# Optimization experiments

Hardware: AMD Instinct MI355X
Metric: run time of the kernel (lower is better)

## Reference

```python
import jax, jax.numpy as jnp
import numpy as np

B, T, V, H = 32, 512, 32000, 1024


def setup_inputs() -> dict:
    key = jax.random.key(0)
    k0, k1, k2, k3 = jax.random.split(key, 4)
    x = jax.random.randint(k0, (B, T), 0, V, dtype=jnp.int32)
    hidden = jnp.zeros((B, H), jnp.float32)
    embedding = jax.random.normal(k1, (V, H), jnp.float32) * 0.02
    # glorot-ish scaling for the gate kernels
    kernel = jax.random.normal(k2, (H, 3 * H), jnp.float32) * (1.0 / np.sqrt(H))
    recurrent_kernel = jax.random.normal(k3, (H, 3 * H), jnp.float32) * (1.0 / np.sqrt(H))
    bias = jnp.zeros((2, 3 * H), jnp.float32)  # [input_bias, recurrent_bias] (reset_after=True)
    return {"x": x, "hidden": hidden, "embedding": embedding,
            "kernel": kernel, "recurrent_kernel": recurrent_kernel, "bias": bias}


def reference(x, hidden, embedding, kernel, recurrent_kernel, bias):
    mask = (x != 0)                      # mask_zero=True: token id 0 is padding
    emb = embedding[x]                   # [B, T, H]
    b_i, b_r = bias[0], bias[1]

    def step(h, inp):
        x_t, m_t = inp                   # x_t: [B, H], m_t: [B]
        gx = x_t @ kernel + b_i          # [B, 3H]
        gh = h @ recurrent_kernel + b_r  # [B, 3H] (reset_after=True)
        xz, xr, xn = jnp.split(gx, 3, axis=-1)
        hz, hr, hn = jnp.split(gh, 3, axis=-1)
        z = jax.nn.sigmoid(xz + hz)
        r = jax.nn.sigmoid(xr + hr)
        hh = jnp.tanh(xn + r * hn)
        h_new = z * h + (1.0 - z) * hh
        # masked steps: carry previous state/output forward
        h_new = jnp.where(m_t[:, None], h_new, h)
        return h_new, h_new

    xs = (jnp.swapaxes(emb, 0, 1), jnp.swapaxes(mask, 0, 1))  # time-major
    state, outs = jax.lax.scan(step, hidden, xs)
    output = jnp.swapaxes(outs, 0, 1)    # [B, T, H]
    return output, state
```

## Files before the change

kernel.cpp:

```cpp
#include <hip/hip_runtime.h>
#include <hip/hip_bf16.h>
#include <math.h>


#define B_  32
#define T_  512
#define H_  1024
#define H3  3072
#define NG  64
#define UPG 16

typedef short short8 __attribute__((ext_vector_type(8)));
typedef float float4_ __attribute__((ext_vector_type(4)));
typedef int   int4_  __attribute__((ext_vector_type(4)));
typedef unsigned short u16;
typedef unsigned long long ull;

__device__ __forceinline__ float bf2f(u16 u) {
  union { unsigned i; float f; } v; v.i = ((unsigned)u) << 16; return v.f;
}
__device__ __forceinline__ u16 f2bf(float f) {
  union { float f; unsigned i; } v; v.f = f;
  unsigned r = v.i + 0x7FFFu + ((v.i >> 16) & 1u);
  return (u16)(r >> 16);
}
__device__ __forceinline__ float ldf(const void* p, size_t i, int f32) {
  return f32 ? ((const float*)p)[i] : bf2f(((const u16*)p)[i]);
}
__device__ __forceinline__ short8 ld8(const void* base, size_t off, int f32) {
  short8 r;
  if (f32) {
    const float* p = (const float*)base + off;
    float4_ a = *(const float4_*)p;
    float4_ b = *(const float4_*)(p + 4);
    r[0]=(short)f2bf(a[0]); r[1]=(short)f2bf(a[1]); r[2]=(short)f2bf(a[2]); r[3]=(short)f2bf(a[3]);
    r[4]=(short)f2bf(b[0]); r[5]=(short)f2bf(b[1]); r[6]=(short)f2bf(b[2]); r[7]=(short)f2bf(b[3]);
  } else {
    r = *(const short8*)((const u16*)base + off);
  }
  return r;
}

__device__ __forceinline__ ull atomLD(const ull* p) {
  return __hip_atomic_load((ull*)p, __ATOMIC_RELAXED, __HIP_MEMORY_SCOPE_AGENT);
}
__device__ __forceinline__ void atomST(ull* p, ull v) {
  __hip_atomic_store(p, v, __ATOMIC_RELAXED, __HIP_MEMORY_SCOPE_AGENT);
}
__device__ __forceinline__ ull packh(unsigned tag, float h0, float h1) {
  return ((ull)tag << 32) | ((ull)f2bf(h1) << 16) | (ull)f2bf(h0);
}

__global__ __launch_bounds__(256) void detect_norm(
    const void* __restrict__ emb, const void* __restrict__ bias,
    int* dflag, float* __restrict__ bias_c) {
  __shared__ int cnt;
  __shared__ int sflag;
  if (threadIdx.x == 0) cnt = 0;
  __syncthreads();
  const unsigned* e = (const unsigned*)emb;
  const unsigned lo = e[threadIdx.x] & 0xFFFFu;
  if (((lo >> 7) & 0xFFu) >= 128u) atomicAdd(&cnt, 1);
  __syncthreads();
  if (threadIdx.x == 0) {
    sflag = (cnt > 32) ? 1 : 0;
    *dflag = sflag;
  }
  __syncthreads();
  const int f32 = sflag;
  for (int i = threadIdx.x; i < 2 * H3; i += 256) bias_c[i] = ldf(bias, i, f32);
}

__global__ __launch_bounds__(256) void transpose_kernel(
    const void* __restrict__ W, const void* __restrict__ R,
    u16* __restrict__ Wt, u16* __restrict__ Rt, const int* dflag) {
  __shared__ u16 tile[32][33];
  const int f32 = *dflag;
  const void* src = blockIdx.z ? R : W;
  u16* dst = blockIdx.z ? Rt : Wt;
  int k0 = blockIdx.x * 32, n0 = blockIdx.y * 32;
  int c = threadIdx.x & 31, r8 = threadIdx.x >> 5;
  for (int rr = r8; rr < 32; rr += 8)
    tile[rr][c] = f2bf(ldf(src, (size_t)(k0 + rr) * H3 + n0 + c, f32));
  __syncthreads();
  for (int rr = r8; rr < 32; rr += 8)
    dst[(size_t)(n0 + rr) * H_ + k0 + c] = tile[c][rr];
}

__global__ __launch_bounds__(256) void gx_gemm(
    const int* __restrict__ x, const void* __restrict__ emb,
    const u16* __restrict__ Wt, const float* __restrict__ bias_c,
    u16* __restrict__ gx, const int* dflag) {
  __shared__ u16 Al[128][72];
  __shared__ u16 Bl[128][72];
  __shared__ int tok[128];
  const int f32 = *dflag;
  const int tid = threadIdx.x;
  const int n0 = blockIdx.x * 128;
  const int t0 = blockIdx.y * 4;
  if (tid < 128) { int b = tid >> 2, dt = tid & 3; tok[tid] = x[b * T_ + t0 + dt]; }
  __syncthreads();
  const int lane = tid & 63, w = tid >> 6;
  const int l = lane & 15, q = lane >> 4;
  const int wm = w >> 1, wn = w & 1;
  float4_ acc[4][4];
  for (int i = 0; i < 4; i++) for (int j = 0; j < 4; j++) acc[i][j] = (float4_)0.0f;
  const int row = tid >> 1, half = tid & 1;
  for (int k0 = 0; k0 < H_; k0 += 64) {
    const size_t offA = (size_t)tok[row] * H_ + k0 + half * 32;
    const u16* srcB = Wt + (size_t)(n0 + row) * H_ + k0 + half * 32;
#pragma unroll
    for (int c = 0; c < 4; c++) {
      *(short8*)&Al[row][half * 32 + c * 8] = ld8(emb, offA + c * 8, f32);
      *(short8*)&Bl[row][half * 32 + c * 8] = *(const short8*)(srcB + c * 8);
    }
    __syncthreads();
#pragma unroll
    for (int ks = 0; ks < 2; ks++) {
      const int kk = ks * 32 + q * 8;
      short8 af[4], bfv[4];
#pragma unroll
      for (int mi = 0; mi < 4; mi++) af[mi] = *(const short8*)&Al[wm * 64 + mi * 16 + l][kk];
#pragma unroll
      for (int ni = 0; ni < 4; ni++) bfv[ni] = *(const short8*)&Bl[wn * 64 + ni * 16 + l][kk];
#pragma unroll
      for (int mi = 0; mi < 4; mi++)
#pragma unroll
        for (int ni = 0; ni < 4; ni++)
          acc[mi][ni] = __builtin_amdgcn_mfma_f32_16x16x32_bf16(af[mi], bfv[ni], acc[mi][ni], 0, 0, 0);
    }
    __syncthreads();
  }
  for (int ni = 0; ni < 4; ni++) {
    const int n = n0 + wn * 64 + ni * 16 + l;
    const float bi = bias_c[n];
    for (int mi = 0; mi < 4; mi++) {
#pragma unroll
      for (int rr = 0; rr < 4; rr++) {
        const int rloc = wm * 64 + mi * 16 + q * 4 + rr;
        const int b = rloc >> 2, dt = rloc & 3;
        gx[((size_t)(t0 + dt) * H3 + n) * B_ + b] = f2bf(acc[mi][ni][rr] + bi);
      }
    }
  }
}

__global__ __launch_bounds__(256, 1) void gru_recur(
    const int* __restrict__ x, const void* __restrict__ hidden,
    const u16* __restrict__ Rt, const float* __restrict__ bias_c,
    const u16* __restrict__ gx, ull* __restrict__ hbuf,
    void* __restrict__ out, const int* dflag) {
  extern __shared__ char smem[];
  u16* Rl = (u16*)smem;
  float* P = (float*)(smem + 99072);
  unsigned* mw = (unsigned*)(smem + 99072 + 50176);
  const int f32o = *dflag;
  const int g = blockIdx.x, tid = threadIdx.x;
  const int lane = tid & 63, w = tid >> 6;
  const int l = lane & 15, q = lane >> 4;
  float* outf = (float*)out;
  u16* outb = (u16*)out;

  for (int i = tid; i < 48 * 128; i += 256) {
    const int cc = i >> 7, ch = i & 127;
    const int c = cc >> 4, u = cc & 15;
    *(short8*)&Rl[cc * 1032 + ch * 8] =
        *(const short8*)(Rt + (size_t)(c * H_ + g * UPG + u) * H_ + ch * 8);
  }
  for (int i = tid; i < 512; i += 256) mw[i] = 0u;
  __syncthreads();
  for (int i = tid; i < B_ * T_; i += 256) {
    const int b = i >> 9, t = i & 511;
    if (x[i] != 0) atomicOr(&mw[t], 1u << b);
  }

  const int b = tid & 31, up = tid >> 5;
  const int col0 = g * UPG + 2 * up;
  float br[2][3], hp[2];
#pragma unroll
  for (int p = 0; p < 2; p++) {
    const int col = col0 + p;
    br[p][0] = bias_c[H3 + col];
    br[p][1] = bias_c[H3 + H_ + col];
    br[p][2] = bias_c[H3 + 2 * H_ + col];
    hp[p] = ldf(hidden, (size_t)b * H_ + col, f32o);
  }
  atomST(&hbuf[16384 + (size_t)(g * 8 + up) * 32 + b], packh(1u, hp[0], hp[1]));
  __syncthreads();

  for (int t = 0; t < T_; t++) {
    float gxv[2][3];
#pragma unroll
    for (int p = 0; p < 2; p++) {
      const int col = col0 + p;
#pragma unroll
      for (int c = 0; c < 3; c++)
        gxv[p][c] = bf2f(gx[((size_t)t * H3 + c * H_ + col) * B_ + b]);
    }

    const ull* hb = hbuf + (size_t)((t + 1) & 1) * 16384;
    const unsigned tg = (unsigned)(t + 1);
    const int jb0 = w * 128 + q * 4;
    ull va[8][8];
#pragma unroll
    for (int kk = 0; kk < 8; kk++) {
      const ull* p = hb + (size_t)(jb0 + kk * 16) * 32 + l;
#pragma unroll
      for (int i = 0; i < 4; i++) {
        va[kk][i]     = atomLD(p + i * 32);
        va[kk][4 + i] = atomLD(p + i * 32 + 16);
      }
    }
    while (1) {
      int anybad = 0;
#pragma unroll
      for (int kk = 0; kk < 8; kk++) {
        int ok = 1;
#pragma unroll
        for (int i = 0; i < 8; i++) ok &= ((unsigned)(va[kk][i] >> 32) == tg);
        if (!__all(ok)) {
          anybad = 1;
          const ull* p = hb + (size_t)(jb0 + kk * 16) * 32 + l;
#pragma unroll
          for (int i = 0; i < 4; i++) {
            va[kk][i]     = atomLD(p + i * 32);
            va[kk][4 + i] = atomLD(p + i * 32 + 16);
          }
        }
      }
      if (!anybad) break;
      __builtin_amdgcn_s_sleep(1);
    }

    float4_ acc[2][3];
#pragma unroll
    for (int mt = 0; mt < 2; mt++)
#pragma unroll
      for (int nt = 0; nt < 3; nt++) acc[mt][nt] = (float4_)0.0f;
#pragma unroll
    for (int kk = 0; kk < 8; kk++) {
      const int k = w * 256 + kk * 32 + q * 8;
      union { int4_ d; short8 s; } ua, ub;
#pragma unroll
      for (int i = 0; i < 4; i++) {
        ua.d[i] = (int)(unsigned)va[kk][i];
        ub.d[i] = (int)(unsigned)va[kk][4 + i];
      }
      const short8 a0 = ua.s, a1 = ub.s;
      const short8 r0 = *(const short8*)&Rl[(0 * 16 + l) * 1032 + k];
      const short8 r1 = *(const short8*)&Rl[(1 * 16 + l) * 1032 + k];
      const short8 r2 = *(const short8*)&Rl[(2 * 16 + l) * 1032 + k];
      acc[0][0] = __builtin_amdgcn_mfma_f32_16x16x32_bf16(a0, r0, acc[0][0], 0, 0, 0);
      acc[0][1] = __builtin_amdgcn_mfma_f32_16x16x32_bf16(a0, r1, acc[0][1], 0, 0, 0);
      acc[0][2] = __builtin_amdgcn_mfma_f32_16x16x32_bf16(a0, r2, acc[0][2], 0, 0, 0);
      acc[1][0] = __builtin_amdgcn_mfma_f32_16x16x32_bf16(a1, r0, acc[1][0], 0, 0, 0);
      acc[1][1] = __builtin_amdgcn_mfma_f32_16x16x32_bf16(a1, r1, acc[1][1], 0, 0, 0);
      acc[1][2] = __builtin_amdgcn_mfma_f32_16x16x32_bf16(a1, r2, acc[1][2], 0, 0, 0);
    }
    float* Pc = P + (t & 1) * 6272;
#pragma unroll
    for (int mt = 0; mt < 2; mt++)
#pragma unroll
      for (int nt = 0; nt < 3; nt++)
#pragma unroll
        for (int rr = 0; rr < 4; rr++)
          Pc[w * 1568 + (mt * 16 + q * 4 + rr) * 49 + nt * 16 + l] = acc[mt][nt][rr];
    __syncthreads();

    const unsigned mword = mw[t];
#pragma unroll
    for (int p = 0; p < 2; p++) {
      const int u = 2 * up + p;
      float hz = 0.f, hr = 0.f, hn = 0.f;
#pragma unroll
      for (int ww = 0; ww < 4; ww++) {
        const float* Pb = Pc + ww * 1568 + b * 49;
        hz += Pb[u]; hr += Pb[16 + u]; hn += Pb[32 + u];
      }
      hz += br[p][0]; hr += br[p][1]; hn += br[p][2];
      const float z = 1.f / (1.f + __expf(-(gxv[p][0] + hz)));
      const float r = 1.f / (1.f + __expf(-(gxv[p][1] + hr)));
      float nn = gxv[p][2] + r * hn;
      nn = fminf(fmaxf(nn, -15.f), 15.f);
      const float e2 = __expf(2.f * nn);
      const float th = (e2 - 1.f) / (e2 + 1.f);
      float hnew = z * hp[p] + (1.f - z) * th;
      if (!((mword >> b) & 1u)) hnew = hp[p];
      hp[p] = hnew;
    }
    atomST(&hbuf[(size_t)(t & 1) * 16384 + (size_t)(g * 8 + up) * 32 + b],
           packh((unsigned)(t + 2), hp[0], hp[1]));
    const size_t oi = ((size_t)b * T_ + t) * H_ + col0;
    if (f32o) {
      __builtin_nontemporal_store(hp[0], outf + oi);
      __builtin_nontemporal_store(hp[1], outf + oi + 1);
    } else {
      const unsigned pw = ((unsigned)f2bf(hp[1]) << 16) | (unsigned)f2bf(hp[0]);
      __builtin_nontemporal_store(pw, (unsigned*)(outb + oi));
    }
  }
  {
    const size_t oi = (size_t)B_ * T_ * H_ + (size_t)b * H_ + col0;
    if (f32o) {
      __builtin_nontemporal_store(hp[0], outf + oi);
      __builtin_nontemporal_store(hp[1], outf + oi + 1);
    } else {
      const unsigned pw = ((unsigned)f2bf(hp[1]) << 16) | (unsigned)f2bf(hp[0]);
      __builtin_nontemporal_store(pw, (unsigned*)(outb + oi));
    }
  }
}

extern "C" void kernel_launch(void* const* d_in, const int* in_sizes, int n_in,
                              void* d_out, int out_size, void* d_ws, size_t ws_size,
                              hipStream_t stream) {
  const int* x       = (const int*)d_in[0];
  const void* hidden = d_in[1];
  const void* emb    = d_in[2];
  const void* W      = d_in[3];
  const void* R      = d_in[4];
  const void* bias   = d_in[5];
  char* ws = (char*)d_ws;
  u16*   gx      = (u16*)ws;
  u16*   Wt      = (u16*)(ws + 100663296);
  u16*   Rt      = (u16*)(ws + 106954752);
  ull*   hbuf    = (ull*)(ws + 113246208);
  int*   dflag   = (int*)(ws + 113508352);
  float* bias_c  = (float*)(ws + 113508608);

  hipLaunchKernelGGL(detect_norm, dim3(1), dim3(256), 0, stream,
                     emb, bias, dflag, bias_c);
  hipLaunchKernelGGL(transpose_kernel, dim3(32, 96, 2), dim3(256), 0, stream,
                     W, R, Wt, Rt, dflag);
  hipLaunchKernelGGL(gx_gemm, dim3(24, 128), dim3(256), 0, stream,
                     x, emb, Wt, bias_c, gx, dflag);
  hipFuncSetAttribute((const void*)gru_recur, hipFuncAttributeMaxDynamicSharedMemorySize, 151296);
  hipLaunchKernelGGL(gru_recur, dim3(NG), dim3(256), 151296, stream,
                     x, hidden, Rt, bias_c, gx, hbuf, d_out, dflag);
}
```

Measured before the change: 3.017 ms.

## Replace per-element tagged hidden-state polling with per-wave epoch flags

Hidden-state exchange between blocks previously used 64-bit words carrying a step tag beside the packed bf16 pair, and each consumer polled all the words it needed. Now the data is stored as plain 32-bit words, and each wave publishes a per-step epoch flag after a waitcnt. Consumers spin on 256 flags before loading the data once. This halves the exchange traffic and simplifies polling, but relies on relaxed-atomic ordering between the data store and the flag store. The P scratch stride also changes from 49 to 50.

```diff
diff --git a/kernel.cpp b/kernel.cpp
--- a/kernel.cpp
+++ b/kernel.cpp
@@ -14,7 +14,7 @@
 typedef float float4_ __attribute__((ext_vector_type(4)));
 typedef int   int4_  __attribute__((ext_vector_type(4)));
 typedef unsigned short u16;
-typedef unsigned long long ull;
+typedef unsigned int u32;
 
 __device__ __forceinline__ float bf2f(u16 u) {
   union { unsigned i; float f; } v; v.i = ((unsigned)u) << 16; return v.f;
@@ -41,19 +41,19 @@
   return r;
 }
 
-__device__ __forceinline__ ull atomLD(const ull* p) {
-  return __hip_atomic_load((ull*)p, __ATOMIC_RELAXED, __HIP_MEMORY_SCOPE_AGENT);
-}
-__device__ __forceinline__ void atomST(ull* p, ull v) {
+__device__ __forceinline__ u32 aload32(const u32* p) {
+  return __hip_atomic_load((u32*)p, __ATOMIC_RELAXED, __HIP_MEMORY_SCOPE_AGENT);
+}
+__device__ __forceinline__ void astore32(u32* p, u32 v) {
   __hip_atomic_store(p, v, __ATOMIC_RELAXED, __HIP_MEMORY_SCOPE_AGENT);
 }
-__device__ __forceinline__ ull packh(unsigned tag, float h0, float h1) {
-  return ((ull)tag << 32) | ((ull)f2bf(h1) << 16) | (ull)f2bf(h0);
+__device__ __forceinline__ u32 pack2(float h0, float h1) {
+  return ((u32)f2bf(h1) << 16) | (u32)f2bf(h0);
 }
 
 __global__ __launch_bounds__(256) void detect_norm(
     const void* __restrict__ emb, const void* __restrict__ bias,
-    int* dflag, float* __restrict__ bias_c) {
+    int* dflag, float* __restrict__ bias_c, u32* __restrict__ ep) {
   __shared__ int cnt;
   __shared__ int sflag;
   if (threadIdx.x == 0) cnt = 0;
@@ -69,6 +69,8 @@
   __syncthreads();
   const int f32 = sflag;
   for (int i = threadIdx.x; i < 2 * H3; i += 256) bias_c[i] = ldf(bias, i, f32);
+  astore32(&ep[threadIdx.x], 0u);
+  astore32(&ep[threadIdx.x + 256], 0u);
 }
 
 __global__ __launch_bounds__(256) void transpose_kernel(
@@ -148,12 +150,12 @@
 __global__ __launch_bounds__(256, 1) void gru_recur(
     const int* __restrict__ x, const void* __restrict__ hidden,
     const u16* __restrict__ Rt, const float* __restrict__ bias_c,
-    const u16* __restrict__ gx, ull* __restrict__ hbuf,
-    void* __restrict__ out, const int* dflag) {
+    const u16* __restrict__ gx, u32* __restrict__ hdat,
+    u32* __restrict__ ep, void* __restrict__ out, const int* dflag) {
   extern __shared__ char smem[];
   u16* Rl = (u16*)smem;
   float* P = (float*)(smem + 99072);
-  unsigned* mw = (unsigned*)(smem + 99072 + 50176);
+  unsigned* mw = (unsigned*)(smem + 99072 + 51200);
   const int f32o = *dflag;
   const int g = blockIdx.x, tid = threadIdx.x;
   const int lane = tid & 63, w = tid >> 6;
@@ -185,7 +187,10 @@
     br[p][2] = bias_c[H3 + 2 * H_ + col];
     hp[p] = ldf(hidden, (size_t)b * H_ + col, f32o);
   }
-  atomST(&hbuf[16384 + (size_t)(g * 8 + up) * 32 + b], packh(1u, hp[0], hp[1]));
+  astore32(&hdat[16384 + (size_t)(g * 8 + up) * 32 + b], pack2(hp[0], hp[1]));
+  __builtin_amdgcn_s_waitcnt(0);
+  __builtin_amdgcn_sched_barrier(0);
+  if ((tid & 63) == 0) astore32(&ep[256 + g * 4 + w], 1u);
   __syncthreads();
 
   for (int t = 0; t < T_; t++) {
@@ -198,38 +203,30 @@
         gxv[p][c] = bf2f(gx[((size_t)t * H3 + c * H_ + col) * B_ + b]);
     }
 
-    const ull* hb = hbuf + (size_t)((t + 1) & 1) * 16384;
-    const unsigned tg = (unsigned)(t + 1);
+    const u32 aw = (u32)(t + 1);
+    const u32* epp = ep + (size_t)((t + 1) & 1) * 256;
+    const int lid = lane;
+    while (1) {
+      u32 e0 = aload32(epp + lid);
+      u32 e1 = aload32(epp + lid + 64);
+      u32 e2 = aload32(epp + lid + 128);
+      u32 e3 = aload32(epp + lid + 192);
+      if (__all(e0 == aw && e1 == aw && e2 == aw && e3 == aw)) break;
+      __builtin_amdgcn_s_sleep(1);
+    }
+    __builtin_amdgcn_sched_barrier(0);
+
+    const u32* hd = hdat + (size_t)((t + 1) & 1) * 16384;
     const int jb0 = w * 128 + q * 4;
-    ull va[8][8];
+    u32 va[8][8];
 #pragma unroll
     for (int kk = 0; kk < 8; kk++) {
-      const ull* p = hb + (size_t)(jb0 + kk * 16) * 32 + l;
+      const u32* p = hd + (size_t)(jb0 + kk * 16) * 32 + l;
 #pragma unroll
       for (int i = 0; i < 4; i++) {
-        va[kk][i]     = atomLD(p + i * 32);
-        va[kk][4 + i] = atomLD(p + i * 32 + 16);
+        va[kk][i]     = aload32(p + i * 32);
+        va[kk][4 + i] = aload32(p + i * 32 + 16);
       }
-    }
-    while (1) {
-      int anybad = 0;
-#pragma unroll
-      for (int kk = 0; kk < 8; kk++) {
-        int ok = 1;
-#pragma unroll
-        for (int i = 0; i < 8; i++) ok &= ((unsigned)(va[kk][i] >> 32) == tg);
-        if (!__all(ok)) {
-          anybad = 1;
-          const ull* p = hb + (size_t)(jb0 + kk * 16) * 32 + l;
-#pragma unroll
-          for (int i = 0; i < 4; i++) {
-            va[kk][i]     = atomLD(p + i * 32);
-            va[kk][4 + i] = atomLD(p + i * 32 + 16);
-          }
-        }
-      }
-      if (!anybad) break;
-      __builtin_amdgcn_s_sleep(1);
     }
 
     float4_ acc[2][3];
@@ -243,8 +240,8 @@
       union { int4_ d; short8 s; } ua, ub;
 #pragma unroll
       for (int i = 0; i < 4; i++) {
-        ua.d[i] = (int)(unsigned)va[kk][i];
-        ub.d[i] = (int)(unsigned)va[kk][4 + i];
+        ua.d[i] = (int)va[kk][i];
+        ub.d[i] = (int)va[kk][4 + i];
       }
       const short8 a0 = ua.s, a1 = ub.s;
       const short8 r0 = *(const short8*)&Rl[(0 * 16 + l) * 1032 + k];
@@ -257,14 +254,14 @@
       acc[1][1] = __builtin_amdgcn_mfma_f32_16x16x32_bf16(a1, r1, acc[1][1], 0, 0, 0);
       acc[1][2] = __builtin_amdgcn_mfma_f32_16x16x32_bf16(a1, r2, acc[1][2], 0, 0, 0);
     }
-    float* Pc = P + (t & 1) * 6272;
+    float* Pc = P + (t & 1) * 6400;
 #pragma unroll
     for (int mt = 0; mt < 2; mt++)
 #pragma unroll
       for (int nt = 0; nt < 3; nt++)
 #pragma unroll
         for (int rr = 0; rr < 4; rr++)
-          Pc[w * 1568 + (mt * 16 + q * 4 + rr) * 49 + nt * 16 + l] = acc[mt][nt][rr];
+          Pc[w * 1600 + (mt * 16 + q * 4 + rr) * 50 + nt * 16 + l] = acc[mt][nt][rr];
     __syncthreads();
 
     const unsigned mword = mw[t];
@@ -274,7 +271,7 @@
       float hz = 0.f, hr = 0.f, hn = 0.f;
 #pragma unroll
       for (int ww = 0; ww < 4; ww++) {
-        const float* Pb = Pc + ww * 1568 + b * 49;
+        const float* Pb = Pc + ww * 1600 + b * 50;
         hz += Pb[u]; hr += Pb[16 + u]; hn += Pb[32 + u];
       }
       hz += br[p][0]; hr += br[p][1]; hn += br[p][2];
@@ -288,8 +285,11 @@
       if (!((mword >> b) & 1u)) hnew = hp[p];
       hp[p] = hnew;
     }
-    atomST(&hbuf[(size_t)(t & 1) * 16384 + (size_t)(g * 8 + up) * 32 + b],
-           packh((unsigned)(t + 2), hp[0], hp[1]));
+    astore32(&hdat[(size_t)(t & 1) * 16384 + (size_t)(g * 8 + up) * 32 + b],
+             pack2(hp[0], hp[1]));
+    __builtin_amdgcn_s_waitcnt(0);
+    __builtin_amdgcn_sched_barrier(0);
+    if ((tid & 63) == 0) astore32(&ep[(size_t)(t & 1) * 256 + g * 4 + w], (u32)(t + 2));
     const size_t oi = ((size_t)b * T_ + t) * H_ + col0;
     if (f32o) {
       __builtin_nontemporal_store(hp[0], outf + oi);
@@ -324,17 +324,18 @@
   u16*   gx      = (u16*)ws;
   u16*   Wt      = (u16*)(ws + 100663296);
   u16*   Rt      = (u16*)(ws + 106954752);
-  ull*   hbuf    = (ull*)(ws + 113246208);
+  u32*   hdat    = (u32*)(ws + 113246208);
+  u32*   ep      = (u32*)(ws + 113246208 + 131072);
   int*   dflag   = (int*)(ws + 113508352);
   float* bias_c  = (float*)(ws + 113508608);
 
   hipLaunchKernelGGL(detect_norm, dim3(1), dim3(256), 0, stream,
-                     emb, bias, dflag, bias_c);
+                     emb, bias, dflag, bias_c, ep);
   hipLaunchKernelGGL(transpose_kernel, dim3(32, 96, 2), dim3(256), 0, stream,
                      W, R, Wt, Rt, dflag);
   hipLaunchKernelGGL(gx_gemm, dim3(24, 128), dim3(256), 0, stream,
                      x, emb, Wt, bias_c, gx, dflag);
-  hipFuncSetAttribute((const void*)gru_recur, hipFuncAttributeMaxDynamicSharedMemorySize, 151296);
-  hipLaunchKernelGGL(gru_recur, dim3(NG), dim3(256), 151296, stream,
-                     x, hidden, Rt, bias_c, gx, hbuf, d_out, dflag);
-}
+  hipFuncSetAttribute((const void*)gru_recur, hipFuncAttributeMaxDynamicSharedMemorySize, 152320);
+  hipLaunchKernelGGL(gru_recur, dim3(NG), dim3(256), 152320, stream,
+                     x, hidden, Rt, bias_c, gx, hdat, ep, d_out, dflag);
+}
```

After: 2.735 ms. 1.1x faster.
